# Optimization experiments

Hardware: AMD Instinct MI355X
Metric: run time of the kernel (lower is better)

Reference implementation:

```python
import jax, jax.numpy as jnp
import numpy as np
import math

B, CIN, COUT, K, G, SD, H = 8, 512, 512, 3, 16, 512, 32
EPS = 1e-8


def _blur_kernel():
    k = jnp.array([1., 3., 3., 1.], dtype=jnp.float32)
    k = k[None, :] * k[:, None]
    k = k / k.sum()
    return k * 4.0  # upsample_factor ** 2


def setup_inputs() -> dict:
    key = jax.random.key(0)
    ks = jax.random.split(key, 10)
    return {
        "x": jax.random.normal(ks[0], (B, CIN, H, H), jnp.float32),
        "co": jax.random.uniform(ks[1], (1, CIN, CIN), jnp.float32),
        "style": jax.random.normal(ks[2], (B, 2 * SD), jnp.float32),
        "noise": jax.random.normal(ks[3], (B, 1, 2 * H, 2 * H), jnp.float32),
        "W": jax.random.normal(ks[4], (1, COUT, CIN, K, K), jnp.float32),
        "mb_w": jax.random.normal(ks[5], (G, SD), jnp.float32),
        "mb_b": jnp.ones((G,), jnp.float32),
        "mod_w": jax.random.normal(ks[6], (CIN, SD), jnp.float32),
        "mod_b": jnp.ones((CIN,), jnp.float32),
        "cluster": jax.random.normal(ks[7], (G, CIN), jnp.float32),
        "gate": -jnp.ones((1,), jnp.float32),
        "tmpr": -2.0 * jnp.ones((1,), jnp.float32),
        "noise_weight": jnp.zeros((1,), jnp.float32),
        "flr_bias": jnp.zeros((COUT,), jnp.float32),
    }


def _l2norm(x, axis):
    n = jnp.linalg.norm(x, axis=axis, keepdims=True)
    return x / jnp.maximum(n, 1e-12)


def reference(x, co, style, noise, W, mb_w, mb_b, mod_w, mod_b,
              cluster, gate, tmpr, noise_weight, flr_bias):
    scale = 1.0 / math.sqrt(CIN * K * K)   # GroupModulatedConv2d.scale
    lin_scale = 1.0 / math.sqrt(SD)        # EqualLinear scale (lr_mul=1)

    t = jax.nn.sigmoid(tmpr) * 5.0
    g = jax.nn.sigmoid(gate)
    S = jax.nn.sigmoid((co - g) * 50.0)                    # (1,Cin,Cin)
    cl = jax.nn.softmax(t * cluster, axis=0)               # (G,Cin)
    loss1 = jnp.sum((cl.T @ cl - jax.lax.stop_gradient(S)) ** 2)
    loss2 = jnp.sum((jnp.float32(CIN * CIN / G) - jnp.sum(S)) ** 2)
    grouped = jax.lax.stop_gradient(jnp.round(jax.nn.softmax(cl * 500.0, axis=0))) + 1e-6

    s1, s2 = style[:, :SD], style[:, SD:]
    style_base = (s1 @ (mb_w * lin_scale).T + mb_b)[:, :, None]   # (B,G,1)
    st = (s2 @ (mod_w * lin_scale).T + mod_b)[:, None, :]         # (B,1,Cin)
    tmp = _l2norm(grouped[None] * st, axis=2)                     # (B,G,Cin)
    st = jnp.sum(tmp * style_base, axis=1)                        # (B,Cin)

    w = scale * W * st[:, None, :, None, None]                    # (B,Cout,Cin,K,K)
    demod = jax.lax.rsqrt(jnp.sum(w * w, axis=(2, 3, 4)) + EPS)   # (B,Cout)
    w = w * demod[:, :, None, None, None]

    # conv_transpose2d(stride=2, pad=0, groups=B) == per-sample conv with
    # lhs_dilation=2, padding=K-1, spatially-flipped kernel.
    wf = w[:, :, :, ::-1, ::-1]

    def per_sample(xi, wi):  # xi (Cin,h,w), wi (Cout,Cin,K,K)
        return jax.lax.conv_general_dilated(
            xi[None], wi, window_strides=(1, 1),
            padding=((K - 1, K - 1), (K - 1, K - 1)), lhs_dilation=(2, 2),
            dimension_numbers=('NCHW', 'OIHW', 'NCHW'))[0]

    out = jax.vmap(per_sample)(x, wf)                             # (B,Cout,65,65)

    # Blur: upfirdn2d, pad=(1,1), depthwise 4x4 symmetric FIR kernel.
    bk = _blur_kernel()
    kdw = jnp.broadcast_to(bk[None, None], (COUT, 1, 4, 4))
    out = jax.lax.conv_general_dilated(
        out, kdw, (1, 1), ((1, 1), (1, 1)), feature_group_count=COUT,
        dimension_numbers=('NCHW', 'OIHW', 'NCHW'))                # (B,Cout,64,64)

    # Correlation of base weights (detached, fed to next layer as `co`).
    wflat = W.reshape(COUT, -1)
    wn = _l2norm(wflat, axis=1)
    co_out = jax.lax.stop_gradient((wn @ wn.T)[None])              # (1,Cout,Cout)

    # NoiseInjection + FusedLeakyReLU
    out = out + noise_weight * noise
    out = jax.nn.leaky_relu(out + flr_bias[None, :, None, None], 0.2) * math.sqrt(2.0)
    return out, co_out, loss1, loss2
```

## Files before the change

### kernel.cpp

```cpp
#include <hip/hip_runtime.h>
#include <hip/hip_bf16.h>

#define NB 8
#define LIN_SCALE 0.044194173824159216f
#define SCALE 0.014731391274719736f

typedef __attribute__((ext_vector_type(8))) short short8;
typedef __attribute__((ext_vector_type(4))) float floatx4;

static constexpr size_t O_XS   = 0;
static constexpr size_t O_OUT1 = 9469952;
static constexpr size_t O_WRT  = 44081152;
static constexpr size_t O_WB   = 48799744;
static constexpr size_t O_PG   = 53518336;
static constexpr size_t O_WSQ  = 61906944;
static constexpr size_t O_CL   = 62955520;
static constexpr size_t O_GR   = O_CL + 32768;
static constexpr size_t O_SB   = O_GR + 32768;
static constexpr size_t O_ST0  = O_SB + 1024;
static constexpr size_t O_STS  = O_ST0 + 16384;
static constexpr size_t O_ST2  = O_STS + 16384;
static constexpr size_t O_WNI  = O_ST2 + 16384;
static constexpr size_t O_DM   = O_WNI + 2048;
static constexpr size_t O_ACC  = O_DM + 16384;

static constexpr size_t OUT_CO = 16777216;
static constexpr size_t OUT_L  = 17039360;

__device__ const int c_ylim[4] = {33,33,32,32};
__device__ const int c_xlim[4] = {33,32,33,32};
__device__ const int c_ntap[4] = {4,2,2,1};
__device__ const int c_tap0[4] = {0,4,6,8};
__device__ const int c_nmb[4]  = {69,66,66,64};
__device__ const int c_cnt[4]  = {276,264,264,256};
__device__ const int c_dy[9] = {-1,-1,0,0, -1,0, 0,0, 0};
__device__ const int c_dx[9] = {-1,0,-1,0, 0,0, -1,0, 0};
__device__ const int c_ky[9] = {2,2,0,0, 2,0, 1,1, 1};
__device__ const int c_kx[9] = {2,0,2,0, 1,1, 2,0, 1};
__device__ const long c_poff[4] = {0, 4460544, 8785920, 13111296};

__device__ __forceinline__ float wave_red(float v) {
#pragma unroll
  for (int s = 32; s > 0; s >>= 1) v += __shfl_down(v, s);
  return v;
}

__device__ __forceinline__ void gl_lds16(const void* g, void* l) {
  __builtin_amdgcn_global_load_lds((const __attribute__((address_space(1))) void*)g,
                                   (__attribute__((address_space(3))) void*)l, 16, 0, 0);
}

__device__ __forceinline__ unsigned short bf16b(float f) {
  union { __hip_bfloat16 h; unsigned short u; } cv;
  cv.h = __float2bfloat16(f);
  return cv.u;
}

__device__ __forceinline__ float bfu(unsigned short u) {
  union { float f; unsigned u32; } c; c.u32 = ((unsigned)u) << 16; return c.f;
}

__device__ __forceinline__ int xcd_chunk(int lb, int cnt) {
  const int q = cnt >> 3, r = cnt & 7;
  const int c = lb & 7, i = lb >> 3;
  return (c < r) ? c*(q+1) + i : r*(q+1) + (c - r)*q + i;
}

__global__ __launch_bounds__(256) void k_big1(const float* __restrict__ W,
    float* __restrict__ wsq, float* __restrict__ wni,
    __hip_bfloat16* __restrict__ wrt, unsigned short* __restrict__ wb,
    const float* __restrict__ style, const float* __restrict__ mod_w,
    const float* __restrict__ mod_b, float* __restrict__ st0,
    const float* __restrict__ co, const float* __restrict__ gate,
    const float* __restrict__ cluster, const float* __restrict__ tmpr,
    const float* __restrict__ mb_w, const float* __restrict__ mb_b,
    float* __restrict__ gr, float* __restrict__ sb,
    float* __restrict__ pacc, __hip_bfloat16* __restrict__ xs) {
  __shared__ float sh[8192];
  __shared__ float extra[8];
  const int bid = blockIdx.x, tid = threadIdx.x;
  const int lane = tid & 63, wv = tid >> 6;
  if (bid < 512) {
    const int o = bid;
    for (int j = tid; j < 4608; j += 256) sh[j] = W[(size_t)o*4608 + j];
    __syncthreads();
    float tot = 0.f;
#pragma unroll
    for (int half = 0; half < 2; half++) {
      const int i = tid + half*256;
      float s = 0.f;
#pragma unroll
      for (int k = 0; k < 9; k++) { float w = sh[i*9 + k]; s = fmaf(w, w, s); }
      wsq[o*512 + i] = s; tot += s;
#pragma unroll
      for (int tp = 0; tp < 9; tp++)
        wrt[((size_t)tp*512 + o)*512 + i] = __float2bfloat16(sh[i*9 + c_ky[tp]*3 + c_kx[tp]]);
    }
    for (int j = tid; j < 4608; j += 256) wb[(size_t)o*4608 + j] = bf16b(sh[j]);
    tot = wave_red(tot);
    if (lane == 0) extra[wv] = tot;
    __syncthreads();
    if (tid == 0) wni[o] = 1.f / fmaxf(sqrtf(extra[0]+extra[1]+extra[2]+extra[3]), 1e-12f);
  } else if (bid < 576) {
    const int b = (bid - 512) >> 3, oc = (bid - 512) & 7;
    sh[tid] = style[b*1024 + 512 + tid];
    sh[tid + 256] = style[b*1024 + 768 + tid];
    __syncthreads();
#pragma unroll
    for (int rr = 0; rr < 16; rr++) {
      const int c = oc*64 + wv*16 + rr;
      const float* mw = mod_w + (size_t)c*512;
      float acc = 0.f;
#pragma unroll
      for (int it = 0; it < 8; it++) acc = fmaf(mw[lane + 64*it], sh[lane + 64*it], acc);
      acc = wave_red(acc);
      if (lane == 0) st0[b*512 + c] = acc*LIN_SCALE + mod_b[c];
    }
  } else if (bid < 1088) {
    const int i = bid - 576;
    const float tt = 5.f / (1.f + expf(-tmpr[0]));
    const float gg = 1.f / (1.f + expf(-gate[0]));
    for (int j = tid; j < 512; j += 256) {
      float v[16]; float m = -1e30f;
#pragma unroll
      for (int g = 0; g < 16; g++) { v[g] = tt * cluster[g*512 + j]; m = fmaxf(m, v[g]); }
      float s = 0.f;
#pragma unroll
      for (int g = 0; g < 16; g++) { v[g] = expf(v[g] - m); s += v[g]; }
      float inv = 1.f / s;
#pragma unroll
      for (int g = 0; g < 16; g++) sh[g*512 + j] = v[g] * inv;
    }
    __syncthreads();
    float cli[16];
#pragma unroll
    for (int k = 0; k < 16; k++) cli[k] = sh[k*512 + i];
    float p1 = 0.f, p2 = 0.f;
    for (int j = tid; j < 512; j += 256) {
      float d = 0.f;
#pragma unroll
      for (int k = 0; k < 16; k++) d = fmaf(cli[k], sh[k*512 + j], d);
      float S = 1.f / (1.f + expf(-50.f*(co[i*512 + j] - gg)));
      float e = d - S;
      p1 = fmaf(e, e, p1); p2 += S;
    }
    p1 = wave_red(p1); p2 = wave_red(p2);
    if (lane == 0) { extra[wv] = p1; extra[4 + wv] = p2; }
    __syncthreads();
    if (tid == 0)  pacc[i]       = extra[0]+extra[1]+extra[2]+extra[3];
    if (tid == 64) pacc[512 + i] = extra[4]+extra[5]+extra[6]+extra[7];
  } else if (bid == 1088) {
    const float tt = 5.f / (1.f + expf(-tmpr[0]));
#pragma unroll
    for (int h = 0; h < 2; h++) {
      const int c = tid + h*256;
      float v[16]; float m = -1e30f;
#pragma unroll
      for (int g = 0; g < 16; g++) { v[g] = tt * cluster[g*512 + c]; m = fmaxf(m, v[g]); }
      float s = 0.f;
#pragma unroll
      for (int g = 0; g < 16; g++) { v[g] = expf(v[g] - m); s += v[g]; }
      float inv = 1.f / s;
      float clv[16]; float m2 = -1e30f;
#pragma unroll
      for (int g = 0; g < 16; g++) { clv[g] = v[g]*inv; m2 = fmaxf(m2, 500.f*clv[g]); }
      float s2 = 0.f; float e2[16];
#pragma unroll
      for (int g = 0; g < 16; g++) { e2[g] = expf(500.f*clv[g] - m2); s2 += e2[g]; }
      float i2 = 1.f / s2;
#pragma unroll
      for (int g = 0; g < 16; g++) gr[g*512 + c] = rintf(e2[g]*i2) + 1e-6f;
    }
    for (int task = wv; task < 128; task += 4) {
      int b = task >> 4, g = task & 15;
      const float* s1 = style + b*1024;
      const float* mw = mb_w + g*512;
      float acc = 0.f;
#pragma unroll
      for (int it = 0; it < 8; it++) acc = fmaf(s1[lane + 64*it], mw[lane + 64*it], acc);
      acc = wave_red(acc);
      if (lane == 0) sb[b*16 + g] = acc*LIN_SCALE + mb_b[g];
    }
  } else {
    const int id0 = (bid - 1089)*256 + tid;
    const float4 z = make_float4(0.f, 0.f, 0.f, 0.f);
    float4* xq = (float4*)xs;
#pragma unroll
    for (int it = 0; it < 22; ++it) {
      const int id = id0 + it*3072;
      const int c = id & 63;
      const int pb = id >> 6;
      const int b = pb / 132;
      const int pix = pb - b*132;
      int y, xx;
      if (pix < 34)       { y = 0;        xx = pix; }
      else if (pix < 68)  { y = 33;       xx = pix - 34; }
      else if (pix < 100) { y = pix - 67; xx = 0; }
      else                { y = pix - 99; xx = 33; }
      xq[((size_t)(b*34 + y)*34 + xx)*64 + c] = z;
    }
  }
}

__global__ __launch_bounds__(256) void k_big2(const float* __restrict__ st0,
    const float* __restrict__ gr, const float* __restrict__ sb,
    const float* __restrict__ wsq, float* __restrict__ dm,
    const float* __restrict__ x, __hip_bfloat16* __restrict__ xs,
    const float* __restrict__ pacc, float* __restrict__ out_tail) {
  __shared__ float L[64*65];
  __shared__ float red[16][4];
  __shared__ float inv[16];
  __shared__ float sbb[16];
  const int tid = threadIdx.x;
  const int lane = tid & 63, wv = tid >> 6;

  if (blockIdx.x == 1088) {
    float a = pacc[tid] + pacc[tid + 256];
    float b2 = pacc[512 + tid] + pacc[768 + tid];
    a = wave_red(a); b2 = wave_red(b2);
    if (lane == 0) { red[0][wv] = a; red[1][wv] = b2; }
    __syncthreads();
    if (tid == 0) {
      float p1 = red[0][0]+red[0][1]+red[0][2]+red[0][3];
      float p2 = red[1][0]+red[1][1]+red[1][2]+red[1][3];
      out_tail[0] = p1;
      float d = 16384.f - p2;
      out_tail[1] = d*d;
    }
    return;
  }

  const int b = (blockIdx.x < 64) ? (blockIdx.x >> 3) : ((blockIdx.x - 64) >> 7);
  float s0 = st0[b*512 + tid], s1 = st0[b*512 + 256 + tid];
  float g0[16], g1[16];
#pragma unroll
  for (int g = 0; g < 16; g++) { g0[g] = gr[g*512 + tid]; g1[g] = gr[g*512 + 256 + tid]; }
#pragma unroll
  for (int g = 0; g < 16; g++) {
    float a = g0[g]*s0, c = g1[g]*s1;
    float p = wave_red(a*a + c*c);
    if (lane == 0) red[g][wv] = p;
  }
  if (tid < 16) sbb[tid] = sb[b*16 + tid];
  __syncthreads();
  if (tid < 16) {
    float ttn = red[tid][0] + red[tid][1] + red[tid][2] + red[tid][3];
    inv[tid] = 1.f / fmaxf(sqrtf(ttn), 1e-12f);
  }
  __syncthreads();
  float f0 = 0.f, f1 = 0.f;
#pragma unroll
  for (int g = 0; g < 16; g++) {
    float w = inv[g]*sbb[g];
    f0 = fmaf(g0[g], w, f0); f1 = fmaf(g1[g], w, f1);
  }
  const float sn0 = s0*f0, sn1 = s1*f1;

  if (blockIdx.x < 64) {
    const int oc = blockIdx.x & 7;
    L[tid] = sn0*sn0;
    L[tid + 256] = sn1*sn1;
    __syncthreads();
#pragma unroll
    for (int rr = 0; rr < 16; rr++) {
      const int o = oc*64 + wv*16 + rr;
      const float* wp = wsq + (size_t)o*512;
      float acc = 0.f;
#pragma unroll
      for (int it = 0; it < 8; it++) acc = fmaf(wp[lane + 64*it], L[lane + 64*it], acc);
      acc = wave_red(acc);
      if (lane == 0) dm[b*512 + o] = rsqrtf((1.0f/4608.0f)*acc + 1e-8f);
    }
    return;
  }

  L[tid] = sn0*SCALE;
  L[tid + 256] = sn1*SCALE;
  __syncthreads();
  const int id = blockIdx.x - 64;
  const int p0 = ((id >> 3) & 15) * 64;
  const int i0 = (id & 7) * 64;
  const int iw = tid & 63, pw = tid >> 6;
  const float sv = L[i0 + iw];
  __syncthreads();
  const int lp = tid & 63, li = tid >> 6;
  const float* xp = x + ((size_t)b*512 + i0)*1024 + p0;
#pragma unroll
  for (int ii = 0; ii < 16; ii++) {
    const int i = li + 4*ii;
    L[i*65 + lp] = xp[(size_t)i*1024 + lp];
  }
  __syncthreads();
#pragma unroll
  for (int pp = 0; pp < 16; pp++) {
    const int pix = p0 + pw + 4*pp;
    const int y = pix >> 5, xq = pix & 31;
    xs[(((size_t)b*34 + (y+1))*34 + (xq+1))*512 + i0 + iw] = __float2bfloat16(L[iw*65 + pw + 4*pp] * sv);
  }
}

__global__ __launch_bounds__(256, 3) void k_mfma(
    const __hip_bfloat16* __restrict__ xs, const __hip_bfloat16* __restrict__ wrt,
    __hip_bfloat16* __restrict__ out1, const __hip_bfloat16* __restrict__ wb,
    float* __restrict__ pgram) {
  __shared__ __hip_bfloat16 smem[24576];
  const int fid = blockIdx.x;
  const int tid = threadIdx.x;
  const int lane = tid & 63, wv = tid >> 6;
  const int wm = (wv >> 1) << 6, wn = (wv & 1) << 6;
  const int col16 = lane & 15, quad = lane >> 4;
  const int colp = col16 ^ ((col16 >> 2) & 1);
  const int soff = (quad ^ (col16 & 3)) << 3;

  int aoff[4], boff[4];
#pragma unroll
  for (int t = 0; t < 4; t++) {
    aoff[t] = (wm + t*16 + colp)*32 + soff;
    boff[t] = 4096 + (wn + t*16 + colp)*32 + soff;
  }
  floatx4 acc[4][4];
#pragma unroll
  for (int i = 0; i < 4; i++)
#pragma unroll
    for (int j = 0; j < 4; j++) acc[i][j] = (floatx4){0.f, 0.f, 0.f, 0.f};

  if (fid >= 276 && fid < 404) {
    const int g = xcd_chunk(fid - 276, 128);
    const int m0 = (g & 3) * 128, n0 = ((g >> 2) & 3) * 128;
    const long kz = (long)(g >> 4) * 576;
    long abase[2], bbase[2]; int ldso[2];
#pragma unroll
    for (int r = 0; r < 2; r++) {
      const int idx = r*256 + tid;
      const int rowp = idx >> 2;
      const int row = rowp ^ ((rowp >> 2) & 1);
      const int kc = (((idx & 3) ^ (row & 3)) << 3);
      abase[r] = (long)(m0 + row)*4608 + kz + kc;
      bbase[r] = (long)(n0 + row)*4608 + kz + kc;
      ldso[r] = idx << 3;
    }
#define STAGE_GRAM(s_) do { \
      const int kk_ = (s_) << 5; \
      const int lo_ = ((s_) % 3) * 8192; \
      gl_lds16(wb + (abase[0] + kk_), smem + lo_ + ldso[0]); \
      gl_lds16(wb + (abase[1] + kk_), smem + lo_ + ldso[1]); \
      gl_lds16(wb + (bbase[0] + kk_), smem + lo_ + 4096 + ldso[0]); \
      gl_lds16(wb + (bbase[1] + kk_), smem + lo_ + 4096 + ldso[1]); \
    } while (0)
    STAGE_GRAM(0);
    STAGE_GRAM(1);
    for (int s = 0; s < 18; ++s) {
      if (s + 1 < 18) asm volatile("s_waitcnt vmcnt(4)\n\ts_barrier" ::: "memory");
      else            asm volatile("s_waitcnt vmcnt(0)\n\ts_barrier" ::: "memory");
      if (s + 2 < 18) STAGE_GRAM(s + 2);
      const int lo = (s % 3) * 8192;
      short8 af[4], bfr[4];
#pragma unroll
      for (int t = 0; t < 4; t++) {
        af[t]  = *(const short8*)(smem + lo + aoff[t]);
        bfr[t] = *(const short8*)(smem + lo + boff[t]);
      }
#pragma unroll
      for (int i = 0; i < 4; i++)
#pragma unroll
        for (int j = 0; j < 4; j++)
          acc[i][j] = __builtin_amdgcn_mfma_f32_16x16x32_bf16(af[i], bfr[j], acc[i][j], 0, 0, 0);
    }
    float* pg = pgram + (size_t)(g >> 4) * 262144;
#pragma unroll
    for (int i = 0; i < 4; i++)
#pragma unroll
      for (int j = 0; j < 4; j++) {
        const int m = m0 + wm + i*16 + (quad << 2);
        const int n = n0 + wn + j*16 + col16;
#pragma unroll
        for (int r = 0; r < 4; r++) pg[(size_t)(m + r)*512 + n] = acc[i][j][r];
      }
    return;
  }

  int cls, lb;
  if (fid < 276)      { cls = 0; lb = fid; }
  else if (fid < 668) { cls = 1; lb = fid - 404; }
  else if (fid < 932) { cls = 2; lb = fid - 668; }
  else                { cls = 3; lb = fid - 932; }
  const int lg = xcd_chunk(lb, c_cnt[cls]);
  const int mb = lg >> 2, nb = lg & 3;
  const int xlim = c_xlim[cls];
  const int npix = c_ylim[cls] * xlim;
  const int M = NB * npix;
  const int m0 = mb * 128, n0 = nb * 128;
  const int t0 = c_tap0[cls];
  const int ntap = c_ntap[cls];

  long abase[2], bbase[2]; int ldso[2];
#pragma unroll
  for (int r = 0; r < 2; r++) {
    const int idx = r*256 + tid;
    const int rowp = idx >> 2;
    const int row = rowp ^ ((rowp >> 2) & 1);
    const int kc = (((idx & 3) ^ (row & 3)) << 3);
    int rm = m0 + row; if (rm >= M) rm = 0;
    const int b = rm / npix; const int rem = rm - b*npix;
    const int yy = rem / xlim; const int xx = rem - yy*xlim;
    abase[r] = ((long)(b*34 + yy + 1)*34 + (xx + 1))*512 + kc;
    bbase[r] = ((long)(t0*512 + n0 + row))*512 + kc;
    ldso[r] = idx << 3;
  }

  const int nst = ntap << 4;
#define STAGE_CONV(s_) do { \
    const int tap_ = t0 + ((s_) >> 4); \
    const long adel_ = (long)((c_dy[tap_]*34 + c_dx[tap_])*512); \
    const long bdel_ = (long)((s_) >> 4) << 18; \
    const int kk_ = ((s_) & 15) << 5; \
    const int lo_ = ((s_) % 3) * 8192; \
    gl_lds16(xs + (abase[0] + adel_ + kk_), smem + lo_ + ldso[0]); \
    gl_lds16(xs + (abase[1] + adel_ + kk_), smem + lo_ + ldso[1]); \
    gl_lds16(wrt + (bbase[0] + bdel_ + kk_), smem + lo_ + 4096 + ldso[0]); \
    gl_lds16(wrt + (bbase[1] + bdel_ + kk_), smem + lo_ + 4096 + ldso[1]); \
  } while (0)
  STAGE_CONV(0);
  STAGE_CONV(1);
  for (int s = 0; s < nst; ++s) {
    if (s + 1 < nst) asm volatile("s_waitcnt vmcnt(4)\n\ts_barrier" ::: "memory");
    else             asm volatile("s_waitcnt vmcnt(0)\n\ts_barrier" ::: "memory");
    if (s + 2 < nst) STAGE_CONV(s + 2);
    const int lo = (s % 3) * 8192;
    short8 af[4], bfr[4];
#pragma unroll
    for (int t = 0; t < 4; t++) {
      af[t]  = *(const short8*)(smem + lo + aoff[t]);
      bfr[t] = *(const short8*)(smem + lo + boff[t]);
    }
#pragma unroll
    for (int i = 0; i < 4; i++)
#pragma unroll
      for (int j = 0; j < 4; j++)
        acc[i][j] = __builtin_amdgcn_mfma_f32_16x16x32_bf16(af[i], bfr[j], acc[i][j], 0, 0, 0);
  }

  __syncthreads();
  __hip_bfloat16* plane = out1 + c_poff[cls];
#pragma unroll
  for (int h = 0; h < 2; h++) {
    if ((wv & 1) == h) {
#pragma unroll
      for (int i = 0; i < 4; i++) {
        const int mrow = wm + i*16 + (quad << 2);
#pragma unroll
        for (int j = 0; j < 4; j++) {
          const int ncl = j*16 + col16;
          ushort4 v;
          v.x = bf16b(acc[i][j][0]); v.y = bf16b(acc[i][j][1]);
          v.z = bf16b(acc[i][j][2]); v.w = bf16b(acc[i][j][3]);
          *(ushort4*)(smem + ncl*138 + mrow) = v;
        }
      }
    }
    __syncthreads();
#pragma unroll
    for (int it = 0; it < 4; it++) {
      const int c = it*256 + tid;
      const int ol = c >> 4, ml = (c & 15) << 3;
      const int mg = m0 + ml;
      if (mg < M) {
        const ushort4 v = *(const ushort4*)(smem + ol*138 + ml);
        *(ushort4*)(plane + (long)(n0 + h*64 + ol)*M + mg) = v;
      }
    }
    __syncthreads();
  }
}

__global__ __launch_bounds__(256) void k_blur(const __hip_bfloat16* __restrict__ out1,
    const float* __restrict__ dm, const float* __restrict__ noise,
    const float* __restrict__ nw, const float* __restrict__ fb, float* __restrict__ out,
    const float* __restrict__ pgram, const float* __restrict__ wni,
    float* __restrict__ co_out) {
  if (blockIdx.x < 256) {
    const int i4 = blockIdx.x*256 + threadIdx.x;
    float4 s = make_float4(0.f, 0.f, 0.f, 0.f);
#pragma unroll
    for (int z = 0; z < 8; z++) {
      const float4 v = ((const float4*)(pgram + (size_t)z*262144))[i4];
      s.x += v.x; s.y += v.y; s.z += v.z; s.w += v.w;
    }
    const float wm = wni[i4 >> 7];
    const float4 wn4 = ((const float4*)wni)[i4 & 127];
    float4 o;
    o.x = s.x*wm*wn4.x; o.y = s.y*wm*wn4.y; o.z = s.z*wm*wn4.z; o.w = s.w*wm*wn4.w;
    ((float4*)co_out)[i4] = o;
    return;
  }
  const int bo = blockIdx.x - 256;
  const int b = bo >> 9, o = bo & 511;
  __shared__ unsigned short L[65 * 68];
  const int tid = threadIdx.x;
  const unsigned short* p0 = (const unsigned short*)out1 + 0        + (long)o * 8712 + b * 1089;
  const unsigned short* p1 = (const unsigned short*)out1 + 4460544  + (long)o * 8448 + b * 1056;
  const unsigned short* p2 = (const unsigned short*)out1 + 8785920  + (long)o * 8448 + b * 1056;
  const unsigned short* p3 = (const unsigned short*)out1 + 13111296 + (long)o * 8192 + b * 1024;
  for (int m = tid; m < 65; m += 256) { L[m*68 + 0] = 0; L[m*68 + 66] = 0; }
  for (int e = tid; e < 1089; e += 256) { int y = e / 33, x = e - 33*y; L[(2*y)*68 + 2*x + 1] = p0[e]; }
  for (int e = tid; e < 1056; e += 256) { int y = e >> 5, x = e & 31;   L[(2*y)*68 + 2*x + 2] = p1[e]; }
  for (int e = tid; e < 1056; e += 256) { int y = e / 33, x = e - 33*y; L[(2*y+1)*68 + 2*x + 1] = p2[e]; }
  for (int e = tid; e < 1024; e += 256) { int y = e >> 5, x = e & 31;   L[(2*y+1)*68 + 2*x + 2] = p3[e]; }
  __syncthreads();
  const float dmv = dm[bo];
  const float nwv = nw[0];
  const float bv = fb[o];
  const int Q = tid & 63;
  const int qy = tid >> 6;
  const int mbase = 16 * qy - 1;
  float hs[18];
#pragma unroll
  for (int rm = 0; rm < 18; rm++) {
    const int m = mbase + rm;
    float s = 0.f;
    if (m >= 0 && m <= 64) {
      const unsigned short* row = L + m*68 + Q;
      s = 0.25f * (bfu(row[0]) + bfu(row[3])) + 0.75f * (bfu(row[1]) + bfu(row[2]));
    }
    hs[rm] = s;
  }
  float* op = out + ((size_t)bo << 12);
  const float* npl = noise + ((size_t)b << 12);
#pragma unroll
  for (int pp = 0; pp < 16; pp++) {
    const int P = 16 * qy + pp;
    float s = 0.25f * (hs[pp] + hs[pp + 3]) + 0.75f * (hs[pp + 1] + hs[pp + 2]);
    float v = fmaf(dmv, s, fmaf(nwv, npl[P * 64 + Q], bv));
    v = (v >= 0.f ? v : 0.2f * v) * 1.4142135623730951f;
    op[P * 64 + Q] = v;
  }
}

extern "C" void kernel_launch(void* const* d_in, const int* in_sizes, int n_in,
                              void* d_out, int out_size, void* d_ws, size_t ws_size,
                              hipStream_t stream) {
  const float* x       = (const float*)d_in[0];
  const float* co      = (const float*)d_in[1];
  const float* style   = (const float*)d_in[2];
  const float* noise   = (const float*)d_in[3];
  const float* W       = (const float*)d_in[4];
  const float* mb_w    = (const float*)d_in[5];
  const float* mb_b    = (const float*)d_in[6];
  const float* mod_w   = (const float*)d_in[7];
  const float* mod_b   = (const float*)d_in[8];
  const float* cluster = (const float*)d_in[9];
  const float* gate    = (const float*)d_in[10];
  const float* tmpr    = (const float*)d_in[11];
  const float* nw      = (const float*)d_in[12];
  const float* fb      = (const float*)d_in[13];
  float* out = (float*)d_out;
  char* ws = (char*)d_ws;

  __hip_bfloat16* xs   = (__hip_bfloat16*)(ws + O_XS);
  __hip_bfloat16* out1 = (__hip_bfloat16*)(ws + O_OUT1);
  __hip_bfloat16* wrt  = (__hip_bfloat16*)(ws + O_WRT);
  __hip_bfloat16* wb   = (__hip_bfloat16*)(ws + O_WB);
  float* pgram = (float*)(ws + O_PG);
  float* wsq = (float*)(ws + O_WSQ);
  float* gr  = (float*)(ws + O_GR);
  float* sb  = (float*)(ws + O_SB);
  float* st0 = (float*)(ws + O_ST0);
  float* wni = (float*)(ws + O_WNI);
  float* dm  = (float*)(ws + O_DM);
  float* pacc = (float*)(ws + O_STS);

  k_big1<<<1101, 256, 0, stream>>>(W, wsq, wni, wrt, (unsigned short*)wb,
                                   style, mod_w, mod_b, st0, co, gate,
                                   cluster, tmpr, mb_w, mb_b, gr, sb, pacc, xs);
  k_big2<<<1089, 256, 0, stream>>>(st0, gr, sb, wsq, dm, x, xs, pacc, out + OUT_L);
  k_mfma<<<1188, 256, 0, stream>>>(xs, wrt, out1, wb, pgram);
  k_blur<<<4352, 256, 0, stream>>>(out1, dm, noise, nw, fb, out, pgram, wni, out + OUT_CO);
}
```

Measured before the change: 240.4 us.

## Vectorize prep and epilogue memory access, rotate LDS stage offsets, raise MFMA priority

The x-scaling prep kernel now loads x with float4 and stores bf16 pairs, and the blur epilogue loads packed ushort2 values. It also stages the horizontal blur pass in a shared float buffer so the vertical pass and output stores can use float4. The GEMM loops replace the modulo-3 buffer offset with rotating counters and wrap the MFMA block in s_setprio to favour math issue. These target narrow global accesses and per-iteration address arithmetic. The cost is extra LDS for the blur and possible misaligned ushort2 access on odd bases.

```diff
diff --git a/kernel.cpp b/kernel.cpp
--- a/kernel.cpp
+++ b/kernel.cpp
@@ -280,22 +280,36 @@
   const int id = blockIdx.x - 64;
   const int p0 = ((id >> 3) & 15) * 64;
   const int i0 = (id & 7) * 64;
-  const int iw = tid & 63, pw = tid >> 6;
-  const float sv = L[i0 + iw];
-  __syncthreads();
-  const int lp = tid & 63, li = tid >> 6;
+  const int iw2 = (tid & 31) * 2, pw = tid >> 5;
+  const float sv0 = L[i0 + iw2];
+  const float sv1 = L[i0 + iw2 + 1];
+  __syncthreads();
+  const int cg = (tid & 15) * 4, ir = tid >> 4;
   const float* xp = x + ((size_t)b*512 + i0)*1024 + p0;
-#pragma unroll
-  for (int ii = 0; ii < 16; ii++) {
-    const int i = li + 4*ii;
-    L[i*65 + lp] = xp[(size_t)i*1024 + lp];
-  }
-  __syncthreads();
-#pragma unroll
-  for (int pp = 0; pp < 16; pp++) {
-    const int pix = p0 + pw + 4*pp;
+  float4 xv[4];
+#pragma unroll
+  for (int ii = 0; ii < 4; ii++) {
+    const int i = ir + 16*ii;
+    xv[ii] = *(const float4*)(xp + (size_t)i*1024 + cg);
+  }
+#pragma unroll
+  for (int ii = 0; ii < 4; ii++) {
+    const int i = ir + 16*ii;
+    L[i*65 + cg + 0] = xv[ii].x;
+    L[i*65 + cg + 1] = xv[ii].y;
+    L[i*65 + cg + 2] = xv[ii].z;
+    L[i*65 + cg + 3] = xv[ii].w;
+  }
+  __syncthreads();
+#pragma unroll
+  for (int pp = 0; pp < 8; pp++) {
+    const int po = pw + 8*pp;
+    const int pix = p0 + po;
     const int y = pix >> 5, xq = pix & 31;
-    xs[(((size_t)b*34 + (y+1))*34 + (xq+1))*512 + i0 + iw] = __float2bfloat16(L[iw*65 + pw + 4*pp] * sv);
+    ushort2 w;
+    w.x = bf16b(L[iw2*65 + po] * sv0);
+    w.y = bf16b(L[(iw2+1)*65 + po] * sv1);
+    *(ushort2*)((unsigned short*)xs + (((size_t)b*34 + (y+1))*34 + (xq+1))*512 + i0 + iw2) = w;
   }
 }
 
@@ -339,32 +353,35 @@
       bbase[r] = (long)(n0 + row)*4608 + kz + kc;
       ldso[r] = idx << 3;
     }
-#define STAGE_GRAM(s_) do { \
+#define STAGE_GRAM(s_, lo_) do { \
       const int kk_ = (s_) << 5; \
-      const int lo_ = ((s_) % 3) * 8192; \
-      gl_lds16(wb + (abase[0] + kk_), smem + lo_ + ldso[0]); \
-      gl_lds16(wb + (abase[1] + kk_), smem + lo_ + ldso[1]); \
-      gl_lds16(wb + (bbase[0] + kk_), smem + lo_ + 4096 + ldso[0]); \
-      gl_lds16(wb + (bbase[1] + kk_), smem + lo_ + 4096 + ldso[1]); \
+      gl_lds16(wb + (abase[0] + kk_), smem + (lo_) + ldso[0]); \
+      gl_lds16(wb + (abase[1] + kk_), smem + (lo_) + ldso[1]); \
+      gl_lds16(wb + (bbase[0] + kk_), smem + (lo_) + 4096 + ldso[0]); \
+      gl_lds16(wb + (bbase[1] + kk_), smem + (lo_) + 4096 + ldso[1]); \
     } while (0)
-    STAGE_GRAM(0);
-    STAGE_GRAM(1);
+    STAGE_GRAM(0, 0);
+    STAGE_GRAM(1, 8192);
+    int loC = 0, loS = 16384;
     for (int s = 0; s < 18; ++s) {
       if (s + 1 < 18) asm volatile("s_waitcnt vmcnt(4)\n\ts_barrier" ::: "memory");
       else            asm volatile("s_waitcnt vmcnt(0)\n\ts_barrier" ::: "memory");
-      if (s + 2 < 18) STAGE_GRAM(s + 2);
-      const int lo = (s % 3) * 8192;
+      if (s + 2 < 18) STAGE_GRAM(s + 2, loS);
       short8 af[4], bfr[4];
 #pragma unroll
       for (int t = 0; t < 4; t++) {
-        af[t]  = *(const short8*)(smem + lo + aoff[t]);
-        bfr[t] = *(const short8*)(smem + lo + boff[t]);
+        af[t]  = *(const short8*)(smem + loC + aoff[t]);
+        bfr[t] = *(const short8*)(smem + loC + boff[t]);
       }
+      __builtin_amdgcn_s_setprio(1);
 #pragma unroll
       for (int i = 0; i < 4; i++)
 #pragma unroll
         for (int j = 0; j < 4; j++)
           acc[i][j] = __builtin_amdgcn_mfma_f32_16x16x32_bf16(af[i], bfr[j], acc[i][j], 0, 0, 0);
+      __builtin_amdgcn_s_setprio(0);
+      loC = (loC == 16384) ? 0 : loC + 8192;
+      loS = (loS == 16384) ? 0 : loS + 8192;
     }
     float* pg = pgram + (size_t)(g >> 4) * 262144;
 #pragma unroll
@@ -409,35 +426,38 @@
   }
 
   const int nst = ntap << 4;
-#define STAGE_CONV(s_) do { \
+#define STAGE_CONV(s_, lo_) do { \
     const int tap_ = t0 + ((s_) >> 4); \
     const long adel_ = (long)((c_dy[tap_]*34 + c_dx[tap_])*512); \
     const long bdel_ = (long)((s_) >> 4) << 18; \
     const int kk_ = ((s_) & 15) << 5; \
-    const int lo_ = ((s_) % 3) * 8192; \
-    gl_lds16(xs + (abase[0] + adel_ + kk_), smem + lo_ + ldso[0]); \
-    gl_lds16(xs + (abase[1] + adel_ + kk_), smem + lo_ + ldso[1]); \
-    gl_lds16(wrt + (bbase[0] + bdel_ + kk_), smem + lo_ + 4096 + ldso[0]); \
-    gl_lds16(wrt + (bbase[1] + bdel_ + kk_), smem + lo_ + 4096 + ldso[1]); \
+    gl_lds16(xs + (abase[0] + adel_ + kk_), smem + (lo_) + ldso[0]); \
+    gl_lds16(xs + (abase[1] + adel_ + kk_), smem + (lo_) + ldso[1]); \
+    gl_lds16(wrt + (bbase[0] + bdel_ + kk_), smem + (lo_) + 4096 + ldso[0]); \
+    gl_lds16(wrt + (bbase[1] + bdel_ + kk_), smem + (lo_) + 4096 + ldso[1]); \
   } while (0)
-  STAGE_CONV(0);
-  STAGE_CONV(1);
+  STAGE_CONV(0, 0);
+  STAGE_CONV(1, 8192);
+  int loC = 0, loS = 16384;
   for (int s = 0; s < nst; ++s) {
     if (s + 1 < nst) asm volatile("s_waitcnt vmcnt(4)\n\ts_barrier" ::: "memory");
     else             asm volatile("s_waitcnt vmcnt(0)\n\ts_barrier" ::: "memory");
-    if (s + 2 < nst) STAGE_CONV(s + 2);
-    const int lo = (s % 3) * 8192;
+    if (s + 2 < nst) STAGE_CONV(s + 2, loS);
     short8 af[4], bfr[4];
 #pragma unroll
     for (int t = 0; t < 4; t++) {
-      af[t]  = *(const short8*)(smem + lo + aoff[t]);
-      bfr[t] = *(const short8*)(smem + lo + boff[t]);
-    }
+      af[t]  = *(const short8*)(smem + loC + aoff[t]);
+      bfr[t] = *(const short8*)(smem + loC + boff[t]);
+    }
+    __builtin_amdgcn_s_setprio(1);
 #pragma unroll
     for (int i = 0; i < 4; i++)
 #pragma unroll
       for (int j = 0; j < 4; j++)
         acc[i][j] = __builtin_amdgcn_mfma_f32_16x16x32_bf16(af[i], bfr[j], acc[i][j], 0, 0, 0);
+    __builtin_amdgcn_s_setprio(0);
+    loC = (loC == 16384) ? 0 : loC + 8192;
+    loS = (loS == 16384) ? 0 : loS + 8192;
   }
 
   __syncthreads();
@@ -496,43 +516,59 @@
   const int bo = blockIdx.x - 256;
   const int b = bo >> 9, o = bo & 511;
   __shared__ unsigned short L[65 * 68];
+  __shared__ float Hs[67 * 64];
   const int tid = threadIdx.x;
   const unsigned short* p0 = (const unsigned short*)out1 + 0        + (long)o * 8712 + b * 1089;
   const unsigned short* p1 = (const unsigned short*)out1 + 4460544  + (long)o * 8448 + b * 1056;
   const unsigned short* p2 = (const unsigned short*)out1 + 8785920  + (long)o * 8448 + b * 1056;
   const unsigned short* p3 = (const unsigned short*)out1 + 13111296 + (long)o * 8192 + b * 1024;
   for (int m = tid; m < 65; m += 256) { L[m*68 + 0] = 0; L[m*68 + 66] = 0; }
+  if (tid < 64) { Hs[tid] = 0.f; Hs[66*64 + tid] = 0.f; }
   for (int e = tid; e < 1089; e += 256) { int y = e / 33, x = e - 33*y; L[(2*y)*68 + 2*x + 1] = p0[e]; }
-  for (int e = tid; e < 1056; e += 256) { int y = e >> 5, x = e & 31;   L[(2*y)*68 + 2*x + 2] = p1[e]; }
+  for (int e2 = tid; e2 < 528; e2 += 256) {
+    const int e = e2*2; const int y = e >> 5, x = e & 31;
+    const ushort2 u = *(const ushort2*)(p1 + e);
+    L[(2*y)*68 + 2*x + 2] = u.x; L[(2*y)*68 + 2*x + 4] = u.y;
+  }
   for (int e = tid; e < 1056; e += 256) { int y = e / 33, x = e - 33*y; L[(2*y+1)*68 + 2*x + 1] = p2[e]; }
-  for (int e = tid; e < 1024; e += 256) { int y = e >> 5, x = e & 31;   L[(2*y+1)*68 + 2*x + 2] = p3[e]; }
+  for (int e2 = tid; e2 < 512; e2 += 256) {
+    const int e = e2*2; const int y = e >> 5, x = e & 31;
+    const ushort2 u = *(const ushort2*)(p3 + e);
+    L[(2*y+1)*68 + 2*x + 2] = u.x; L[(2*y+1)*68 + 2*x + 4] = u.y;
+  }
+  __syncthreads();
+  for (int e = tid; e < 4160; e += 256) {
+    const int m = e >> 6, q = e & 63;
+    const unsigned short* row = L + m*68 + q;
+    Hs[(m+1)*64 + q] = 0.25f * (bfu(row[0]) + bfu(row[3])) + 0.75f * (bfu(row[1]) + bfu(row[2]));
+  }
   __syncthreads();
   const float dmv = dm[bo];
   const float nwv = nw[0];
   const float bv = fb[o];
-  const int Q = tid & 63;
-  const int qy = tid >> 6;
-  const int mbase = 16 * qy - 1;
-  float hs[18];
-#pragma unroll
-  for (int rm = 0; rm < 18; rm++) {
-    const int m = mbase + rm;
-    float s = 0.f;
-    if (m >= 0 && m <= 64) {
-      const unsigned short* row = L + m*68 + Q;
-      s = 0.25f * (bfu(row[0]) + bfu(row[3])) + 0.75f * (bfu(row[1]) + bfu(row[2]));
-    }
-    hs[rm] = s;
-  }
+  const int qx = (tid & 15) << 2;
+  const int py = tid >> 4;
   float* op = out + ((size_t)bo << 12);
   const float* npl = noise + ((size_t)b << 12);
 #pragma unroll
-  for (int pp = 0; pp < 16; pp++) {
-    const int P = 16 * qy + pp;
-    float s = 0.25f * (hs[pp] + hs[pp + 3]) + 0.75f * (hs[pp + 1] + hs[pp + 2]);
-    float v = fmaf(dmv, s, fmaf(nwv, npl[P * 64 + Q], bv));
-    v = (v >= 0.f ? v : 0.2f * v) * 1.4142135623730951f;
-    op[P * 64 + Q] = v;
+  for (int pp = 0; pp < 4; pp++) {
+    const int P = py + (pp << 4);
+    const float4 h0 = *(const float4*)(Hs + (P    )*64 + qx);
+    const float4 h1 = *(const float4*)(Hs + (P + 1)*64 + qx);
+    const float4 h2 = *(const float4*)(Hs + (P + 2)*64 + qx);
+    const float4 h3 = *(const float4*)(Hs + (P + 3)*64 + qx);
+    const float4 n4 = *(const float4*)(npl + P*64 + qx);
+    float4 ov;
+    float s;
+    s = 0.25f*(h0.x + h3.x) + 0.75f*(h1.x + h2.x);
+    ov.x = fmaf(dmv, s, fmaf(nwv, n4.x, bv)); ov.x = (ov.x >= 0.f ? ov.x : 0.2f*ov.x) * 1.4142135623730951f;
+    s = 0.25f*(h0.y + h3.y) + 0.75f*(h1.y + h2.y);
+    ov.y = fmaf(dmv, s, fmaf(nwv, n4.y, bv)); ov.y = (ov.y >= 0.f ? ov.y : 0.2f*ov.y) * 1.4142135623730951f;
+    s = 0.25f*(h0.z + h3.z) + 0.75f*(h1.z + h2.z);
+    ov.z = fmaf(dmv, s, fmaf(nwv, n4.z, bv)); ov.z = (ov.z >= 0.f ? ov.z : 0.2f*ov.z) * 1.4142135623730951f;
+    s = 0.25f*(h0.w + h3.w) + 0.75f*(h1.w + h2.w);
+    ov.w = fmaf(dmv, s, fmaf(nwv, n4.w, bv)); ov.w = (ov.w >= 0.f ? ov.w : 0.2f*ov.w) * 1.4142135623730951f;
+    *(float4*)(op + P*64 + qx) = ov;
   }
 }
 
```

Result: no change. 239.5 us (-0.4%).
